# Kernel tuning notes

Hardware: AMD Instinct MI355X
Metric: run time of the kernel (lower is better)

The kernel has to match this reference:

```python
import jax, jax.numpy as jnp
import numpy as np

DIM = 1024
NUM_EXPERTS = 4
NUM_HEADS = 16
MLP_RATIO = 4
B, N = 8, 1024
EPS = 1e-5


def layernorm(x, w, b):
    mu = jnp.mean(x, axis=-1, keepdims=True)
    var = jnp.mean(jnp.square(x - mu), axis=-1, keepdims=True)
    return (x - mu) * jax.lax.rsqrt(var + EPS) * w + b


def setup_inputs() -> dict:
    key = jax.random.key(0)
    ks = jax.random.split(key, 6)
    x = jax.random.normal(ks[0], (B, N, DIM), dtype=jnp.float32)
    expert_mask = jax.random.randint(ks[1], (B, N), 0, NUM_EXPERTS)
    expert_probs = jax.random.uniform(ks[2], (B, N), dtype=jnp.float32)
    expand_dim = 3 * DIM + MLP_RATIO * DIM
    expand_weight = jax.random.normal(ks[3], (expand_dim, DIM), dtype=jnp.float32) * 0.02
    mlp_bias = jnp.zeros((MLP_RATIO * DIM,), dtype=jnp.float32)
    contract_weight = jax.random.normal(ks[4], (2 * DIM, MLP_RATIO * DIM + DIM), dtype=jnp.float32) * 0.02
    contract_bias = jnp.zeros((2 * DIM,), dtype=jnp.float32)
    norm1_w = jnp.ones((DIM,), dtype=jnp.float32)
    norm1_b = jnp.zeros((DIM,), dtype=jnp.float32)
    norm2_w = jnp.ones((2 * DIM,), dtype=jnp.float32)
    norm2_b = jnp.zeros((2 * DIM,), dtype=jnp.float32)
    return {"x": x, "expert_probs": expert_probs, "expand_weight": expand_weight,
            "mlp_bias": mlp_bias, "contract_weight": contract_weight,
            "contract_bias": contract_bias, "norm1_w": norm1_w, "norm1_b": norm1_b,
            "norm2_w": norm2_w, "norm2_b": norm2_b, "expert_mask": expert_mask}


def reference(x, expert_probs, expand_weight, mlp_bias, contract_weight,
              contract_bias, norm1_w, norm1_b, norm2_w, norm2_b, expert_mask):
    dim = DIM
    # nested sub-dim per token: expert m uses first dim >> (E-1-m) features
    shift = NUM_EXPERTS - 1 - expert_mask                       # (B, N)
    d_in = dim // jnp.left_shift(1, shift)                      # (B, N)
    in_mask = (jnp.arange(dim)[None, None, :] < d_in[..., None]).astype(x.dtype)

    # fused expand bias: [mlp_bias, qkv_bias(=zeros since qkv_bias=False)]
    input_bias = jnp.concatenate([mlp_bias, jnp.zeros((3 * dim,), x.dtype)], axis=-1)

    xn = layernorm(x, norm1_w, norm1_b) * in_mask               # nested_linear_expand input masking
    y = jnp.einsum('bnd,ed->bne', xn, expand_weight) + input_bias  # (B, N, 7*dim)

    qkv, mlp_hidden = y[..., :3 * dim], y[..., 3 * dim:]
    q = qkv[..., :dim]
    kv = layernorm(qkv[..., dim:], norm2_w, norm2_b)            # (B, N, 2*dim)
    k, v = kv[..., :dim], kv[..., dim:]

    # multi-head attention
    dh = dim // NUM_HEADS
    scale = dh ** -0.5
    b, n = x.shape[0], x.shape[1]
    def heads(t):
        return t.reshape(b, n, NUM_HEADS, dh).transpose(0, 2, 1, 3)
    qh, kh, vh = heads(q), heads(k), heads(v)
    attn = jax.nn.softmax(jnp.einsum('bhqd,bhkd->bhqk', qh, kh) * scale, axis=-1)
    attn_output = jnp.einsum('bhqk,bhkd->bhqd', attn, vh).transpose(0, 2, 1, 3).reshape(b, n, dim)

    # nested_linear_contract: full matmul, then mask outputs beyond (2*dim)>>shift
    concat_in = jnp.concatenate([jax.nn.gelu(mlp_hidden, approximate=False), attn_output], axis=-1)
    cy = jnp.einsum('bnc,oc->bno', concat_in, contract_weight) + contract_bias  # (B, N, 2*dim)
    d_out = (2 * dim) // jnp.left_shift(1, shift)
    out_mask = (jnp.arange(2 * dim)[None, None, :] < d_out[..., None]).astype(x.dtype)
    cy = cy * out_mask + jnp.concatenate([x, x], axis=-1)       # residual.repeat(1,1,2)

    mlp_output, attn_out = cy[..., :dim], cy[..., dim:]
    return attn_out + expert_probs[..., None] * mlp_output
```

## Files before the change

kernel.cpp:

```cpp
#include <hip/hip_runtime.h>
#include <cmath>

#define NT    8192
#define DIM_  1024
#define EXP_  7168
#define CD_   5120
#define OD_   2048
#define MPAD  8704
#define NRT   68

typedef __attribute__((ext_vector_type(8))) short short8;
typedef __attribute__((ext_vector_type(4))) float f32x4;
typedef __attribute__((ext_vector_type(4))) unsigned short ushort4_t;

__device__ __forceinline__ unsigned short f2bf(float f) {
  union { float f; unsigned u; } v; v.f = f;
  return (unsigned short)((v.u + 0x7FFFu + ((v.u >> 16) & 1u)) >> 16);
}
__device__ __forceinline__ float bf2f(unsigned short u) {
  union { unsigned u; float f; } v; v.u = ((unsigned)u) << 16;
  return v.f;
}

#define MFMA16(a, b, c) __builtin_amdgcn_mfma_f32_16x16x32_bf16(a, b, c, 0, 0, 0)

__global__ __launch_bounds__(256) void count_experts(const int* __restrict__ em,
                                                     int* __restrict__ blockCnt) {
  __shared__ int h[4];
  int tid = threadIdx.x;
  if (tid < 4) h[tid] = 0;
  __syncthreads();
  atomicAdd(&h[em[blockIdx.x * 256 + tid]], 1);
  __syncthreads();
  if (tid < 4) blockCnt[blockIdx.x * 4 + tid] = h[tid];
}

__global__ void scan_make(const int* __restrict__ blockCnt, int* __restrict__ desc) {
  if (threadIdx.x != 0) return;
  int cnt[4] = {0, 0, 0, 0};
  for (int b = 0; b < 32; b++)
    for (int e = 0; e < 4; e++) cnt[e] += blockCnt[b * 4 + e];
  int base[4]; int acc = 0;
  for (int e = 0; e < 4; e++) { base[e] = acc; acc += ((cnt[e] + 127) >> 7) << 7; }
  for (int e = 0; e < 4; e++) { desc[e] = base[e]; desc[4 + e] = cnt[e]; }
  for (int r = 0; r < NRT; r++) {
    int te = -1;
    for (int e = 0; e < 4; e++) {
      int lo = base[e] >> 7;
      int hi = (base[e] + (((cnt[e] + 127) >> 7) << 7)) >> 7;
      if (r >= lo && r < hi) te = e;
    }
    desc[8 + r] = te;
  }
  int run[4];
  for (int e = 0; e < 4; e++) run[e] = base[e];
  for (int b = 0; b < 32; b++)
    for (int e = 0; e < 4; e++) { desc[76 + b * 4 + e] = run[e]; run[e] += blockCnt[b * 4 + e]; }
}

__global__ __launch_bounds__(256) void fill_perm(int* __restrict__ perm) {
  int i = blockIdx.x * 256 + threadIdx.x;
  if (i < MPAD) perm[i] = -1;
}

__global__ __launch_bounds__(256) void scatter_perm(const int* __restrict__ em,
    const int* __restrict__ desc, int* __restrict__ perm, int* __restrict__ pos) {
  __shared__ int wsum[4][4];
  int tid = threadIdx.x;
  int wv = tid >> 6, ln = tid & 63;
  int t = blockIdx.x * 256 + tid;
  int e = em[t];
  int wrank = 0;
#pragma unroll
  for (int k = 0; k < 4; k++) {
    unsigned long long m = __ballot(e == k);
    if (ln == 0) wsum[wv][k] = __popcll(m);
    if (e == k) wrank = __popcll(m & ((1ull << ln) - 1ull));
  }
  __syncthreads();
  int off = desc[76 + blockIdx.x * 4 + e];
  for (int w = 0; w < wv; w++) off += wsum[w][e];
  int p = off + wrank;
  perm[p] = t;
  pos[t] = p;
}

__global__ __launch_bounds__(256) void cvt_bf16(const float* __restrict__ in,
                                                unsigned short* __restrict__ out, int n) {
  int i = (blockIdx.x * 256 + threadIdx.x) * 4;
  if (i >= n) return;
  float4 v = *(const float4*)(in + i);
  ushort4_t o;
  o[0] = f2bf(v.x); o[1] = f2bf(v.y); o[2] = f2bf(v.z); o[3] = f2bf(v.w);
  *(ushort4_t*)(out + i) = o;
}

__global__ __launch_bounds__(256) void ln1_kernel(const float* __restrict__ x,
    const float* __restrict__ w, const float* __restrict__ b,
    const int* __restrict__ emask, const int* __restrict__ pos,
    unsigned short* __restrict__ xn) {
  int wave = threadIdx.x >> 6, lane = threadIdx.x & 63;
  int t = blockIdx.x * 4 + wave;
  const float* xt = x + (size_t)t * DIM_;
  float4 v[4];
  float s = 0.f, s2 = 0.f;
#pragma unroll
  for (int i = 0; i < 4; i++) {
    v[i] = *(const float4*)(xt + i * 256 + lane * 4);
    s  += v[i].x + v[i].y + v[i].z + v[i].w;
    s2 += v[i].x * v[i].x + v[i].y * v[i].y + v[i].z * v[i].z + v[i].w * v[i].w;
  }
#pragma unroll
  for (int o = 1; o < 64; o <<= 1) { s += __shfl_xor(s, o); s2 += __shfl_xor(s2, o); }
  float mu = s * (1.f / 1024.f);
  float rs = rsqrtf(s2 * (1.f / 1024.f) - mu * mu + 1e-5f);
  int din = 1024 >> (3 - emask[t]);
  unsigned short* ot = xn + (size_t)pos[t] * DIM_;
#pragma unroll
  for (int i = 0; i < 4; i++) {
    int c0 = i * 256 + lane * 4;
    float fv[4] = { v[i].x, v[i].y, v[i].z, v[i].w };
    ushort4_t o;
#pragma unroll
    for (int j = 0; j < 4; j++) {
      int c = c0 + j;
      float val = (c < din) ? (fv[j] - mu) * rs * w[c] + b[c] : 0.f;
      o[j] = f2bf(val);
    }
    *(ushort4_t*)(ot + c0) = o;
  }
}

__global__ __launch_bounds__(256, 3) void gemm_grp1(
    const unsigned short* __restrict__ A, const unsigned short* __restrict__ W,
    const float* __restrict__ bias, const int* __restrict__ tdesc,
    const int* __restrict__ perm, unsigned short* __restrict__ out0,
    unsigned short* __restrict__ out1, unsigned short* __restrict__ out2) {
  __shared__ unsigned short lds[16384];
  unsigned short* As = lds;
  unsigned short* Bs = lds + 8192;
  const int r = blockIdx.y;
  const int e = tdesc[8 + r];
  if (e < 0) return;
  const int ntiles = 4 << e;
  constexpr int KK = 1024;

  const int tid = threadIdx.x;
  const int lane = tid & 63;
  const int wave = tid >> 6;
  const int wm = wave >> 1, wn = wave & 1;
  const int lg = lane >> 4, lr = lane & 15;

  constexpr int CPX = 56 >> 3;
  const int bx = (int)blockIdx.x;
  const int bn = (bx & 7) * CPX + (bx >> 3);
  const int n0 = bn * 128;
  const int m0 = r * 128;

  const int s0g = tid >> 3,        s1g = (256 + tid) >> 3;
  const int lc0 = (tid & 7) ^ (s0g & 7), lc1 = (tid & 7) ^ (s1g & 7);
  const int row0 = 2 * s0g + (lc0 >> 2), kc0 = lc0 & 3;
  const int row1 = 2 * s1g + (lc1 >> 2), kc1 = lc1 & 3;
  const unsigned short* aS0 = A + (size_t)(m0 + row0) * KK + kc0 * 8;
  const unsigned short* aS1 = A + (size_t)(m0 + row1) * KK + kc1 * 8;
  const unsigned short* bS0 = W + (size_t)(n0 + row0) * KK + kc0 * 8;
  const unsigned short* bS1 = W + (size_t)(n0 + row1) * KK + kc1 * 8;

#define GLD(SRC, DST)                                                                \
  __builtin_amdgcn_global_load_lds(                                                  \
      (const __attribute__((address_space(1))) void*)(SRC),                          \
      (__attribute__((address_space(3))) void*)(DST), 16, 0, 0)
#define STAGE(T, SLOT) {                                                             \
    GLD(aS0 + (size_t)(T) * 32, As + (SLOT) * 4096 + tid * 8);                       \
    GLD(aS1 + (size_t)(T) * 32, As + (SLOT) * 4096 + 2048 + tid * 8);                \
    GLD(bS0 + (size_t)(T) * 32, Bs + (SLOT) * 4096 + tid * 8);                       \
    GLD(bS1 + (size_t)(T) * 32, Bs + (SLOT) * 4096 + 2048 + tid * 8);                \
  }

  const int fb = (lr >> 1) * 128 + ((((lr & 1) << 2) + lg) ^ ((lr >> 1) & 7)) * 16;
  const char* apb = (const char*)As + wm * 4096 + fb;
  const char* bpb = (const char*)Bs + wn * 4096 + fb;

  short8 afr[4], bfr[4];
#define LDFRAG(C)                                                                    \
  _Pragma("unroll") for (int mi = 0; mi < 4; mi++)                                   \
    afr[mi] = *(const short8*)(apb + (C) * 8192 + mi * 1024);                        \
  _Pragma("unroll") for (int ni = 0; ni < 4; ni++)                                   \
    bfr[ni] = *(const short8*)(bpb + (C) * 8192 + ni * 1024);

  f32x4 acc[4][4];
  f32x4 zf = { 0.f, 0.f, 0.f, 0.f };
#pragma unroll
  for (int i = 0; i < 4; i++)
#pragma unroll
    for (int j = 0; j < 4; j++) acc[i][j] = zf;

  STAGE(0, 0)
  STAGE(1, 1)
  asm volatile("s_waitcnt vmcnt(4)" ::: "memory");
  __builtin_amdgcn_s_barrier();

#pragma unroll 1
  for (int t = 0; t < ntiles; ++t) {
    const int c = t & 1;
    LDFRAG(c)
    asm volatile("s_waitcnt lgkmcnt(0)" ::: "memory");
    __builtin_amdgcn_sched_barrier(0);
    __builtin_amdgcn_s_barrier();
    const int t2 = (t + 2 < ntiles) ? t + 2 : t;
    STAGE(t2, c)
    __builtin_amdgcn_s_setprio(1);
#pragma unroll
    for (int mi = 0; mi < 4; mi++)
#pragma unroll
      for (int ni = 0; ni < 4; ni++)
        acc[mi][ni] = MFMA16(afr[mi], bfr[ni], acc[mi][ni]);
    __builtin_amdgcn_s_setprio(0);
    asm volatile("s_waitcnt vmcnt(4)" ::: "memory");
    __builtin_amdgcn_s_barrier();
  }
  asm volatile("s_waitcnt vmcnt(0)" ::: "memory");

#pragma unroll
  for (int mi = 0; mi < 4; mi++) {
#pragma unroll
    for (int ni = 0; ni < 4; ni++) {
#pragma unroll
      for (int rr = 0; rr < 4; rr++) {
        int grow = m0 + wm * 64 + mi * 16 + lg * 4 + rr;
        int gcol = n0 + wn * 64 + ni * 16 + lr;
        float v = acc[mi][ni][rr];
        int tk = perm[grow];
        if (tk < 0) continue;
        float bv = bias[gcol & 4095];
        v += (gcol < 4096) ? bv : 0.f;
        if (gcol < 1024) {
          int bb = tk >> 10, n = tk & 1023, h = gcol >> 6, d = gcol & 63;
          out0[(((size_t)(bb * 16 + h) * 1024 + n) << 6) + d] = f2bf(v * 0.125f);
        } else if (gcol < 3072) {
          out1[(size_t)tk * OD_ + (gcol - 1024)] = f2bf(v);
        } else {
          float g = 0.5f * v * (1.f + erff(v * 0.70710678f));
          out2[(size_t)tk * CD_ + (gcol - 3072)] = f2bf(g);
        }
      }
    }
  }
#undef GLD
#undef STAGE
#undef LDFRAG
}

__global__ __launch_bounds__(512, 2) void gemm2_8p(
    const unsigned short* __restrict__ A, const unsigned short* __restrict__ W,
    const float* __restrict__ bias, unsigned short* __restrict__ out0) {
  extern __shared__ unsigned short lds[];
  unsigned short* As = lds;
  unsigned short* Bs = lds + 32768;
  constexpr int KK = 5120;
  constexpr int NTILES = KK / 64;
  const int tid = threadIdx.x;
  const int lane = tid & 63;
  const int wave = tid >> 6;
  const int wm = wave >> 2;
  const int wn = wave & 3;
  const int lg = lane >> 4, lr = lane & 15;

  int cpx = (int)gridDim.x >> 3;
  int lid = ((int)blockIdx.x & 7) * cpx + ((int)blockIdx.x >> 3);
  int bm = lid >> 3, bn = lid & 7;
  int m0 = bm * 256, n0 = bn * 256;

  const int srow = tid >> 3;
  const int schunk = (tid & 7) ^ (srow & 7);
  const unsigned short* aSrc = A + (size_t)(m0 + srow) * KK + schunk * 8;
  const unsigned short* bSrc = W + (size_t)(n0 + srow) * KK + schunk * 8;

  const int xor0 = (lg ^ (lr & 7)) * 8;
  const int xor1 = ((4 + lg) ^ (lr & 7)) * 8;
  const unsigned short* ap0 = As + (wm * 64 + lr) * 64 + xor0;
  const unsigned short* ap1 = As + (wm * 64 + lr) * 64 + xor1;
  const unsigned short* bp0 = Bs + (wn * 32 + lr) * 64 + xor0;
  const unsigned short* bp1 = Bs + (wn * 32 + lr) * 64 + xor1;

#define STAGE_A(TT, SLOT, SEG)                                                       \
  __builtin_amdgcn_global_load_lds(                                                  \
    (const __attribute__((address_space(1))) void*)(aSrc +                           \
      (size_t)(SEG) * 64 * KK + (size_t)(TT) * 64),                                  \
    (__attribute__((address_space(3))) void*)(As + (SLOT) * 16384 +                  \
      (SEG) * 4096 + tid * 8), 16, 0, 0)
#define STAGE_B(TT, SLOT, SEG)                                                       \
  __builtin_amdgcn_global_load_lds(                                                  \
    (const __attribute__((address_space(1))) void*)(bSrc +                           \
      (size_t)(SEG) * 64 * KK + (size_t)(TT) * 64),                                  \
    (__attribute__((address_space(3))) void*)(Bs + (SLOT) * 16384 +                  \
      (SEG) * 4096 + tid * 8), 16, 0, 0)

  short8 afr[4][2], bfr[2][2][2];
#define LDFRAG_A(C, QM)                                                              \
  _Pragma("unroll") for (int mi = 0; mi < 4; mi++) {                                 \
    afr[mi][0] = *(const short8*)(ap0 + (C) * 16384 + (QM) * 8192 + mi * 1024);      \
    afr[mi][1] = *(const short8*)(ap1 + (C) * 16384 + (QM) * 8192 + mi * 1024);      \
  }
#define LDFRAG_B(C, QN)                                                              \
  _Pragma("unroll") for (int ni = 0; ni < 2; ni++) {                                 \
    bfr[QN][ni][0] = *(const short8*)(bp0 + (C) * 16384 + (QN) * 8192 + ni * 1024);  \
    bfr[QN][ni][1] = *(const short8*)(bp1 + (C) * 16384 + (QN) * 8192 + ni * 1024);  \
  }
#define DOMFMA(QM, QN)                                                               \
  __builtin_amdgcn_s_setprio(1);                                                     \
  _Pragma("unroll") for (int mi = 0; mi < 4; mi++)                                   \
  _Pragma("unroll") for (int ni = 0; ni < 2; ni++) {                                 \
    acc[(QM) * 4 + mi][(QN) * 2 + ni] =                                              \
        MFMA16(afr[mi][0], bfr[QN][ni][0], acc[(QM) * 4 + mi][(QN) * 2 + ni]);       \
    acc[(QM) * 4 + mi][(QN) * 2 + ni] =                                              \
        MFMA16(afr[mi][1], bfr[QN][ni][1], acc[(QM) * 4 + mi][(QN) * 2 + ni]);       \
  }                                                                                  \
  __builtin_amdgcn_s_setprio(0);

#define SCHED0 __builtin_amdgcn_sched_barrier(0)

#define TILE_BODY(T, C) {                                                            \
    const int tn1 = ((T) + 1 < NTILES) ? (T) + 1 : NTILES - 1;                       \
    const int tn2 = ((T) + 2 < NTILES) ? (T) + 2 : NTILES - 1;                       \
    LDFRAG_A(C, 0); LDFRAG_B(C, 0);                                                  \
    STAGE_B(tn1, (C) ^ 1, 2); STAGE_B(tn1, (C) ^ 1, 3);                              \
    SCHED0;                                                                          \
    __builtin_amdgcn_s_barrier();                                                    \
    asm volatile("s_waitcnt lgkmcnt(0)");                                            \
    SCHED0;                                                                          \
    DOMFMA(0, 0);                                                                    \
    asm volatile("s_waitcnt vmcnt(6)" ::: "memory");                                 \
    __builtin_amdgcn_s_barrier();                                                    \
    LDFRAG_B(C, 1);                                                                  \
    STAGE_A(tn1, (C) ^ 1, 2); STAGE_A(tn1, (C) ^ 1, 3);                              \
    SCHED0;                                                                          \
    __builtin_amdgcn_s_barrier();                                                    \
    asm volatile("s_waitcnt lgkmcnt(0)");                                            \
    SCHED0;                                                                          \
    DOMFMA(0, 1);                                                                    \
    __builtin_amdgcn_s_barrier();                                                    \
    LDFRAG_A(C, 1);                                                                  \
    STAGE_A(tn2, (C), 0); STAGE_A(tn2, (C), 1);                                      \
    SCHED0;                                                                          \
    __builtin_amdgcn_s_barrier();                                                    \
    asm volatile("s_waitcnt lgkmcnt(0)");                                            \
    SCHED0;                                                                          \
    DOMFMA(1, 0);                                                                    \
    __builtin_amdgcn_s_barrier();                                                    \
    STAGE_B(tn2, (C), 0); STAGE_B(tn2, (C), 1);                                      \
    SCHED0;                                                                          \
    __builtin_amdgcn_s_barrier();                                                    \
    DOMFMA(1, 1);                                                                    \
    asm volatile("s_waitcnt vmcnt(8)" ::: "memory");                                 \
    __builtin_amdgcn_s_barrier();                                                    \
  }

  f32x4 acc[8][4];
  f32x4 zf = { 0.f, 0.f, 0.f, 0.f };
#pragma unroll
  for (int i = 0; i < 8; i++)
#pragma unroll
    for (int j = 0; j < 4; j++) acc[i][j] = zf;

  STAGE_A(0, 0, 0); STAGE_A(0, 0, 1); STAGE_A(0, 0, 2); STAGE_A(0, 0, 3);
  STAGE_B(0, 0, 0); STAGE_B(0, 0, 1); STAGE_B(0, 0, 2); STAGE_B(0, 0, 3);
  STAGE_A(1, 1, 0); STAGE_A(1, 1, 1);
  STAGE_B(1, 1, 0); STAGE_B(1, 1, 1);
  asm volatile("s_waitcnt vmcnt(4)" ::: "memory");
  __builtin_amdgcn_s_barrier();

#pragma unroll 1
  for (int tp = 0; tp < NTILES / 2; ++tp) {
    TILE_BODY(2 * tp, 0)
    TILE_BODY(2 * tp + 1, 1)
  }
  asm volatile("s_waitcnt vmcnt(0)" ::: "memory");

#pragma unroll
  for (int mi8 = 0; mi8 < 8; mi8++) {
#pragma unroll
    for (int nj = 0; nj < 4; nj++) {
#pragma unroll
      for (int r = 0; r < 4; r++) {
        int grow = m0 + wm * 64 + (mi8 >> 2) * 128 + (mi8 & 3) * 16 + lg * 4 + r;
        int gcol = n0 + wn * 32 + (nj >> 1) * 128 + (nj & 1) * 16 + lr;
        float v = acc[mi8][nj][r] + bias[gcol];
        out0[(size_t)grow * OD_ + gcol] = f2bf(v);
      }
    }
  }
#undef STAGE_A
#undef STAGE_B
#undef LDFRAG_A
#undef LDFRAG_B
#undef DOMFMA
#undef SCHED0
#undef TILE_BODY
}

__global__ __launch_bounds__(256) void ln2_kernel(const unsigned short* __restrict__ kv,
    const float* __restrict__ w, const float* __restrict__ b,
    unsigned short* __restrict__ kb, unsigned short* __restrict__ vrm) {
  int wave = threadIdx.x >> 6, lane = threadIdx.x & 63;
  int t = blockIdx.x * 4 + wave;
  const unsigned short* p = kv + (size_t)t * OD_;
  float vals[4][8];
  float s = 0.f, s2 = 0.f;
#pragma unroll
  for (int i = 0; i < 4; i++) {
    short8 v = *(const short8*)(p + i * 512 + lane * 8);
#pragma unroll
    for (int j = 0; j < 8; j++) {
      float f = bf2f((unsigned short)v[j]);
      vals[i][j] = f; s += f; s2 += f * f;
    }
  }
#pragma unroll
  for (int o = 1; o < 64; o <<= 1) { s += __shfl_xor(s, o); s2 += __shfl_xor(s2, o); }
  float mu = s * (1.f / 2048.f);
  float rs = rsqrtf(s2 * (1.f / 2048.f) - mu * mu + 1e-5f);
  int bidx = t >> 10, n = t & 1023;
#pragma unroll
  for (int i = 0; i < 4; i++) {
    int c0 = i * 512 + lane * 8;
    short8 o8;
#pragma unroll
    for (int j = 0; j < 8; j++) {
      int c = c0 + j;
      o8[j] = (short)f2bf((vals[i][j] - mu) * rs * w[c] + b[c]);
    }
    if (c0 < 1024) {
      int h = c0 >> 6, d = c0 & 63;
      *(short8*)(kb + (((size_t)(bidx * 16 + h) * 1024 + n) << 6) + d) = o8;
    } else {
      *(short8*)(vrm + (size_t)t * 1024 + (c0 - 1024)) = o8;
    }
  }
}

__global__ __launch_bounds__(256) void transpose_v(const unsigned short* __restrict__ vrm,
                                                   unsigned short* __restrict__ vt) {
  int bh = blockIdx.x >> 4;
  int nblk = (blockIdx.x & 15) * 64;
  int b = bh >> 4, h = bh & 15;
  __shared__ unsigned short tile[64][65];
  int tid = threadIdx.x;
  int i = tid >> 2;
  int d0 = (tid & 3) * 16;
  const unsigned short* src = vrm + ((size_t)(b * 1024 + nblk + i)) * 1024 + h * 64 + d0;
  short8 v0 = *(const short8*)(src);
  short8 v1 = *(const short8*)(src + 8);
#pragma unroll
  for (int j = 0; j < 8; j++) {
    tile[d0 + j][i] = (unsigned short)v0[j];
    tile[d0 + 8 + j][i] = (unsigned short)v1[j];
  }
  __syncthreads();
  int d = tid >> 2;
  int i0 = (tid & 3) * 16;
  unsigned short* dst = vt + ((size_t)bh * 64 + d) * 1024 + nblk + i0;
  short8 o0, o1;
#pragma unroll
  for (int j = 0; j < 8; j++) { o0[j] = (short)tile[d][i0 + j]; o1[j] = (short)tile[d][i0 + 8 + j]; }
  *(short8*)dst = o0;
  *(short8*)(dst + 8) = o1;
}

__global__ __launch_bounds__(256) void attn_kernel(const unsigned short* __restrict__ q,
    const unsigned short* __restrict__ k, const unsigned short* __restrict__ vt,
    unsigned short* __restrict__ concat) {
  int bh = blockIdx.x >> 3;
  int wv = threadIdx.x >> 6;
  int q0 = (blockIdx.x & 7) * 128 + wv * 32;
  int lane = threadIdx.x & 63;
  int lg = lane >> 4, lr = lane & 15;
  __shared__ unsigned short plds[4][2][512];
  unsigned short* pw = &plds[wv][0][0];
  const unsigned short* qp = q + (size_t)bh * (1024 * 64);
  const unsigned short* kp = k + (size_t)bh * (1024 * 64);
  const unsigned short* vp = vt + (size_t)bh * (64 * 1024);
  short8 qf[2][2];
#pragma unroll
  for (int rb = 0; rb < 2; rb++)
#pragma unroll
    for (int c = 0; c < 2; c++)
      qf[rb][c] = *(const short8*)(qp + (q0 + rb * 16 + lr) * 64 + c * 32 + lg * 8);
  f32x4 zf = { 0.f, 0.f, 0.f, 0.f };
  f32x4 o[2][4];
  float m[2][4], l[2][4];
#pragma unroll
  for (int rb = 0; rb < 2; rb++) {
#pragma unroll
    for (int r = 0; r < 4; r++) { m[rb][r] = -1e30f; l[rb][r] = 0.f; }
#pragma unroll
    for (int nb = 0; nb < 4; nb++) o[rb][nb] = zf;
  }
  const int prd = lr * 32 + (((lg + lr) & 3) << 3);
  for (int kt = 0; kt < 1024; kt += 32) {
    f32x4 s[2][2];
    s[0][0] = zf; s[0][1] = zf; s[1][0] = zf; s[1][1] = zf;
#pragma unroll
    for (int h2 = 0; h2 < 2; h2++) {
      short8 kf0 = *(const short8*)(kp + (kt + h2 * 16 + lr) * 64 + lg * 8);
      short8 kf1 = *(const short8*)(kp + (kt + h2 * 16 + lr) * 64 + 32 + lg * 8);
      s[0][h2] = MFMA16(qf[0][0], kf0, s[0][h2]);
      s[0][h2] = MFMA16(qf[0][1], kf1, s[0][h2]);
      s[1][h2] = MFMA16(qf[1][0], kf0, s[1][h2]);
      s[1][h2] = MFMA16(qf[1][1], kf1, s[1][h2]);
    }
#pragma unroll
    for (int rb = 0; rb < 2; rb++) {
      float mx[4], rsum[4];
#pragma unroll
      for (int r = 0; r < 4; r++) mx[r] = fmaxf(s[rb][0][r], s[rb][1][r]);
#pragma unroll
      for (int ofs = 1; ofs < 16; ofs <<= 1)
#pragma unroll
        for (int r = 0; r < 4; r++) mx[r] = fmaxf(mx[r], __shfl_xor(mx[r], ofs));
      bool need = false;
#pragma unroll
      for (int r = 0; r < 4; r++) need |= (mx[r] > m[rb][r] + 8.f);
      if (need) {
#pragma unroll
        for (int r = 0; r < 4; r++) {
          float mn = fmaxf(m[rb][r], mx[r]);
          float al = __expf(m[rb][r] - mn);
          m[rb][r] = mn;
          l[rb][r] *= al;
#pragma unroll
          for (int nb = 0; nb < 4; nb++) o[rb][nb][r] *= al;
        }
      }
#pragma unroll
      for (int r = 0; r < 4; r++) {
        float p0 = __expf(s[rb][0][r] - m[rb][r]);
        float p1 = __expf(s[rb][1][r] - m[rb][r]);
        int q_ = lg * 4 + r;
        pw[rb * 512 + q_ * 32 + ((((lr >> 3) + q_) & 3) << 3) + (lr & 7)] = f2bf(p0);
        pw[rb * 512 + q_ * 32 + (((2 + (lr >> 3) + q_) & 3) << 3) + (lr & 7)] = f2bf(p1);
        rsum[r] = p0 + p1;
      }
#pragma unroll
      for (int ofs = 1; ofs < 16; ofs <<= 1)
#pragma unroll
        for (int r = 0; r < 4; r++) rsum[r] += __shfl_xor(rsum[r], ofs);
#pragma unroll
      for (int r = 0; r < 4; r++) l[rb][r] += rsum[r];
    }
    asm volatile("s_waitcnt lgkmcnt(0)" ::: "memory");
    short8 pf0 = *(const short8*)(pw + prd);
    short8 pf1 = *(const short8*)(pw + 512 + prd);
#pragma unroll
    for (int nb = 0; nb < 4; nb++) {
      short8 vf = *(const short8*)(vp + (nb * 16 + lr) * 1024 + kt + lg * 8);
      o[0][nb] = MFMA16(pf0, vf, o[0][nb]);
      o[1][nb] = MFMA16(pf1, vf, o[1][nb]);
    }
  }
  int b = bh >> 4, h = bh & 15;
#pragma unroll
  for (int rb = 0; rb < 2; rb++)
#pragma unroll
    for (int r = 0; r < 4; r++) {
      int n = q0 + rb * 16 + lg * 4 + r;
      size_t t = (size_t)b * 1024 + n;
      float inv = 1.f / l[rb][r];
#pragma unroll
      for (int nb = 0; nb < 4; nb++)
        concat[t * CD_ + 4096 + h * 64 + nb * 16 + lr] = f2bf(o[rb][nb][r] * inv);
    }
}

__global__ __launch_bounds__(256) void final_epi(const unsigned short* __restrict__ cy,
    const float* __restrict__ x, const float* __restrict__ probs,
    const int* __restrict__ emask, float* __restrict__ out) {
  int t = blockIdx.x;
  int c = threadIdx.x * 4;
  int dout = 2048 >> (3 - emask[t]);
  float p = probs[t];
  const unsigned short* cyt = cy + (size_t)t * OD_;
  ushort4_t mv = *(const ushort4_t*)(cyt + c);
  ushort4_t av = *(const ushort4_t*)(cyt + 1024 + c);
  float4 xv = *(const float4*)(x + (size_t)t * 1024 + c);
  float xa[4] = { xv.x, xv.y, xv.z, xv.w };
  float4 o;
  float oa[4];
#pragma unroll
  for (int j = 0; j < 4; j++) {
    float mlp = ((c + j) < dout ? bf2f(mv[j]) : 0.f) + xa[j];
    float att = ((1024 + c + j) < dout ? bf2f(av[j]) : 0.f) + xa[j];
    oa[j] = att + p * mlp;
  }
  o.x = oa[0]; o.y = oa[1]; o.z = oa[2]; o.w = oa[3];
  *(float4*)(out + (size_t)t * 1024 + c) = o;
}

extern "C" void kernel_launch(void* const* d_in, const int* in_sizes, int n_in,
                              void* d_out, int out_size, void* d_ws, size_t ws_size,
                              hipStream_t stream) {
  const float* x        = (const float*)d_in[0];
  const float* probs    = (const float*)d_in[1];
  const float* we       = (const float*)d_in[2];
  const float* mlp_bias = (const float*)d_in[3];
  const float* wc       = (const float*)d_in[4];
  const float* cbias    = (const float*)d_in[5];
  const float* n1w      = (const float*)d_in[6];
  const float* n1b      = (const float*)d_in[7];
  const float* n2w      = (const float*)d_in[8];
  const float* n2b      = (const float*)d_in[9];
  const int*   emask    = (const int*)d_in[10];
  float* out = (float*)d_out;

  char* ws = (char*)d_ws;
  size_t off = 0;
  auto alloc = [&](size_t bytes) {
    char* p = ws + off;
    off += (bytes + 255) & ~(size_t)255;
    return p;
  };
  unsigned short* we_bf = (unsigned short*)alloc((size_t)EXP_ * DIM_ * 2);
  unsigned short* wc_bf = (unsigned short*)alloc((size_t)OD_ * CD_ * 2);
  unsigned short* xn    = (unsigned short*)alloc((size_t)MPAD * DIM_ * 2);
  unsigned short* qb    = (unsigned short*)alloc((size_t)NT * DIM_ * 2);
  unsigned short* kv    = (unsigned short*)alloc((size_t)NT * OD_ * 2);
  unsigned short* kb    = (unsigned short*)alloc((size_t)NT * DIM_ * 2);
  unsigned short* vt    = (unsigned short*)alloc((size_t)NT * DIM_ * 2);
  unsigned short* cc    = (unsigned short*)alloc((size_t)NT * CD_ * 2);
  int* blockCnt         = (int*)alloc(32 * 4 * 4);
  int* desc             = (int*)alloc(256 * 4);
  int* perm             = (int*)alloc(MPAD * 4);
  int* pos              = (int*)alloc(NT * 4);
  unsigned short* vrm = xn;
  unsigned short* cy  = kv;
  if (off > ws_size) return;

  hipFuncSetAttribute((const void*)gemm2_8p,
                      hipFuncAttributeMaxDynamicSharedMemorySize, 131072);

  count_experts<<<32, 256, 0, stream>>>(emask, blockCnt);
  scan_make<<<1, 64, 0, stream>>>(blockCnt, desc);
  fill_perm<<<34, 256, 0, stream>>>(perm);
  scatter_perm<<<32, 256, 0, stream>>>(emask, desc, perm, pos);

  cvt_bf16<<<7168, 256, 0, stream>>>(we, we_bf, EXP_ * DIM_);
  cvt_bf16<<<10240, 256, 0, stream>>>(wc, wc_bf, OD_ * CD_);
  ln1_kernel<<<2048, 256, 0, stream>>>(x, n1w, n1b, emask, pos, xn);
  gemm_grp1<<<dim3(56, NRT), 256, 0, stream>>>(xn, we_bf, mlp_bias, desc,
                                               perm, qb, kv, cc);
  ln2_kernel<<<2048, 256, 0, stream>>>(kv, n2w, n2b, kb, vrm);
  transpose_v<<<2048, 256, 0, stream>>>(vrm, vt);
  attn_kernel<<<1024, 256, 0, stream>>>(qb, kb, vt, cc);
  gemm2_8p<<<256, 512, 131072, stream>>>(cc, wc_bf, cbias, cy);
  final_epi<<<8192, 256, 0, stream>>>(cy, x, probs, emask, out);
}
```

Measured before the change: 506.1 us.

## Software-pipeline K/V global loads in attention loop with MFMA priority boosts

Restructures the flash-attention inner loop to prefetch the next K tile during softmax and to issue V loads at the top of each iteration, using explicit vmcnt waits so memory latency overlaps compute. It also wraps the MFMA bursts in s_setprio to favour matrix issue, and disables unrolling of the main loop. The aim is to hide global-load latency in the attention kernel, at the cost of extra live registers and hand-placed waitcnt assumptions that depend on compiler instruction ordering.

```diff
diff --git a/kernel.cpp b/kernel.cpp
--- a/kernel.cpp
+++ b/kernel.cpp
@@ -497,17 +497,45 @@
     for (int nb = 0; nb < 4; nb++) o[rb][nb] = zf;
   }
   const int prd = lr * 32 + (((lg + lr) & 3) << 3);
+  const unsigned short* kb0 = kp + (size_t)lr * 64 + lg * 8;
+  const unsigned short* kb1 = kp + (size_t)(16 + lr) * 64 + lg * 8;
+  const unsigned short* vb0 = vp + (size_t)(lr) * 1024 + lg * 8;
+  const unsigned short* vb1 = vp + (size_t)(16 + lr) * 1024 + lg * 8;
+  const unsigned short* vb2 = vp + (size_t)(32 + lr) * 1024 + lg * 8;
+  const unsigned short* vb3 = vp + (size_t)(48 + lr) * 1024 + lg * 8;
+
+  short8 kc0, kc1, kc2, kc3;
+  short8 vc0, vc1, vc2, vc3;
+  kc0 = *(const short8*)(kb0);
+  kc1 = *(const short8*)(kb0 + 32);
+  kc2 = *(const short8*)(kb1);
+  kc3 = *(const short8*)(kb1 + 32);
+
+#pragma unroll 1
   for (int kt = 0; kt < 1024; kt += 32) {
+    vc0 = *(const short8*)(vb0 + kt);
+    vc1 = *(const short8*)(vb1 + kt);
+    vc2 = *(const short8*)(vb2 + kt);
+    vc3 = *(const short8*)(vb3 + kt);
+    asm volatile("s_waitcnt vmcnt(4)" ::: "memory");
     f32x4 s[2][2];
     s[0][0] = zf; s[0][1] = zf; s[1][0] = zf; s[1][1] = zf;
-#pragma unroll
-    for (int h2 = 0; h2 < 2; h2++) {
-      short8 kf0 = *(const short8*)(kp + (kt + h2 * 16 + lr) * 64 + lg * 8);
-      short8 kf1 = *(const short8*)(kp + (kt + h2 * 16 + lr) * 64 + 32 + lg * 8);
-      s[0][h2] = MFMA16(qf[0][0], kf0, s[0][h2]);
-      s[0][h2] = MFMA16(qf[0][1], kf1, s[0][h2]);
-      s[1][h2] = MFMA16(qf[1][0], kf0, s[1][h2]);
-      s[1][h2] = MFMA16(qf[1][1], kf1, s[1][h2]);
+    __builtin_amdgcn_s_setprio(1);
+    s[0][0] = MFMA16(qf[0][0], kc0, s[0][0]);
+    s[0][0] = MFMA16(qf[0][1], kc1, s[0][0]);
+    s[1][0] = MFMA16(qf[1][0], kc0, s[1][0]);
+    s[1][0] = MFMA16(qf[1][1], kc1, s[1][0]);
+    s[0][1] = MFMA16(qf[0][0], kc2, s[0][1]);
+    s[0][1] = MFMA16(qf[0][1], kc3, s[0][1]);
+    s[1][1] = MFMA16(qf[1][0], kc2, s[1][1]);
+    s[1][1] = MFMA16(qf[1][1], kc3, s[1][1]);
+    __builtin_amdgcn_s_setprio(0);
+    {
+      const size_t ktn = (kt + 32 < 1024) ? (size_t)(kt + 32) : (size_t)kt;
+      kc0 = *(const short8*)(kb0 + ktn * 64);
+      kc1 = *(const short8*)(kb0 + ktn * 64 + 32);
+      kc2 = *(const short8*)(kb1 + ktn * 64);
+      kc3 = *(const short8*)(kb1 + ktn * 64 + 32);
     }
 #pragma unroll
     for (int rb = 0; rb < 2; rb++) {
@@ -551,12 +579,17 @@
     asm volatile("s_waitcnt lgkmcnt(0)" ::: "memory");
     short8 pf0 = *(const short8*)(pw + prd);
     short8 pf1 = *(const short8*)(pw + 512 + prd);
-#pragma unroll
-    for (int nb = 0; nb < 4; nb++) {
-      short8 vf = *(const short8*)(vp + (nb * 16 + lr) * 1024 + kt + lg * 8);
-      o[0][nb] = MFMA16(pf0, vf, o[0][nb]);
-      o[1][nb] = MFMA16(pf1, vf, o[1][nb]);
-    }
+    asm volatile("s_waitcnt vmcnt(4)" ::: "memory");
+    __builtin_amdgcn_s_setprio(1);
+    o[0][0] = MFMA16(pf0, vc0, o[0][0]);
+    o[1][0] = MFMA16(pf1, vc0, o[1][0]);
+    o[0][1] = MFMA16(pf0, vc1, o[0][1]);
+    o[1][1] = MFMA16(pf1, vc1, o[1][1]);
+    o[0][2] = MFMA16(pf0, vc2, o[0][2]);
+    o[1][2] = MFMA16(pf1, vc2, o[1][2]);
+    o[0][3] = MFMA16(pf0, vc3, o[0][3]);
+    o[1][3] = MFMA16(pf1, vc3, o[1][3]);
+    __builtin_amdgcn_s_setprio(0);
   }
   int b = bh >> 4, h = bh & 15;
 #pragma unroll
```

Result: faster. 494.2 us (-2.4%).
